# Optimization experiments

Measured on AMD Instinct MI355X. Metric: run time of the kernel, lower is better.

The kernel has to match this reference:

```python
import jax, jax.numpy as jnp
import numpy as np

EPS = 1e-10


def setup_inputs() -> dict:
    key = jax.random.key(0)
    k1, k2, k3 = jax.random.split(key, 3)
    B, c = 65536, 64
    xyz = jax.random.normal(k1, (B, 3, 1), dtype=jnp.float32)          # group centers
    xyz_group = xyz + 0.1 * jax.random.normal(k2, (B, 3, c), dtype=jnp.float32)  # neighbor points
    r_lrf = 0.2 + 0.8 * jax.random.uniform(k3, (B,), dtype=jnp.float32)  # per-group support radius
    return {"xyz": xyz, "xyz_group": xyz_group, "r_lrf": r_lrf}


def reference(xyz, xyz_group, r_lrf):
    # xyz: [B,3,1] center; xyz_group: [B,3,c] neighbors; r_lrf: [B]
    B, _, c = xyz_group.shape
    x = xyz - xyz_group                                   # [B,3,c]
    xxt = jnp.einsum('bic,bjc->bij', x, x) / c            # [B,3,3] covariance
    _, _, vh = jnp.linalg.svd(xxt)                        # vh: [B,3,3]
    v_last = vh[:, -1, :]                                 # [B,3] smallest singular vector (torch v[...,-1])

    # sign disambiguation (no-grad in the original)
    center_proj = jnp.einsum('bi,bic->bc', v_last, x)     # [B,c]
    sum_ = (center_proj > 0.001).sum(-1) - (center_proj < -0.001).sum(-1)  # [B]
    sign = jax.lax.stop_gradient(1.0 - 2.0 * (sum_ < 0).astype(jnp.float32))  # [B]

    zp = sign[:, None] * v_last                           # [B,3] z axis
    x = -x                                                # x *= -1 in original
    norm = jnp.einsum('bi,bic->bc', zp, x)                # [B,c] projection onto zp
    vi = x - zp[:, :, None] * norm[:, None, :]            # [B,3,c] in-plane component
    x_l2 = jnp.sqrt(jnp.sum(x * x, axis=1))               # [B,c]
    alpha = (r_lrf[:, None] - x_l2) ** 2                  # [B,c]
    beta = norm * norm                                    # [B,c]
    vi_c = jnp.einsum('bc,bic->bi', alpha * beta, vi)     # [B,3] weighted sum
    xp = vi_c / (jnp.sqrt(jnp.sum(vi_c * vi_c, axis=1, keepdims=True)) + EPS)  # [B,3] x axis
    yp = jnp.cross(xp, zp)                                # [B,3] y axis
    lrf = jnp.stack([xp, yp, zp], axis=2)                 # [B,3,3] columns = axes
    out = jnp.einsum('bij,bic->bjc', lrf, (xyz_group - xyz) / r_lrf[:, None, None])  # lrf^T @ _out_xp
    return out


if __name__ == '__main__':
    o = reference(**setup_inputs())
    print(o.shape)
```

## Files before the change

### kernel.cpp

```cpp
#include <hip/hip_runtime.h>


#define DEVFN static __device__ __forceinline__


DEVFN float slapy2f(float x, float y) {
#pragma clang fp contract(off)
  float xa = fabsf(x), ya = fabsf(y);
  float w = fmaxf(xa, ya);
  float z = fminf(xa, ya);
  if (z == 0.0f) return w;
  float q = z / w;
  return w * sqrtf(fmaf(q, q, 1.0f));
}

DEVFN float snrm2_2f(float a, float b) {
  double da = (double)a, db = (double)b;
  return (float)sqrt(da * da + db * db);
}

DEVFN void slartgf(float f, float g, float &cs, float &sn, float &r) {
#pragma clang fp contract(off)
  if (g == 0.0f) { cs = 1.0f; sn = 0.0f; r = f; return; }
  if (f == 0.0f) { cs = 0.0f; sn = copysignf(1.0f, g); r = fabsf(g); return; }
  float f1 = fabsf(f), g1 = fabsf(g);
  const float rtmin = 0x1p-63f;
  const float rtmax = 6.5219089e18f;
  if (f1 > rtmin && f1 < rtmax && g1 > rtmin && g1 < rtmax) {
    float d = sqrtf(fmaf(f, f, g * g));
    cs = f1 / d;
    r = copysignf(d, f);
    sn = g / r;
  } else {
    const float safmin = 0x1p-126f;
    const float safmax = 0x1p+126f;
    float u = fminf(safmax, fmaxf(safmin, fmaxf(f1, g1)));
    float fs = f / u, gs = g / u;
    float d = sqrtf(fmaf(fs, fs, gs * gs));
    cs = fabsf(fs) / d;
    r = copysignf(d, f);
    sn = gs / r;
    r = r * u;
  }
}

DEVFN void slas2f(float f, float g, float h, float &ssmin, float &ssmax) {
#pragma clang fp contract(off)
  float fa = fabsf(f), ga = fabsf(g), ha = fabsf(h);
  float fhmn = fminf(fa, ha), fhmx = fmaxf(fa, ha);
  if (fhmn == 0.0f) {
    ssmin = 0.0f;
    if (fhmx == 0.0f) {
      ssmax = ga;
    } else {
      float mx = fmaxf(fhmx, ga), mn = fminf(fhmx, ga);
      float q = mn / mx;
      ssmax = mx * sqrtf(fmaf(q, q, 1.0f));
    }
  } else {
    if (ga < fhmx) {
      float as = 1.0f + fhmn / fhmx;
      float at = (fhmx - fhmn) / fhmx;
      float qq = ga / fhmx;
      float au = qq * qq;
      float c = 2.0f / (sqrtf(fmaf(as, as, au)) + sqrtf(fmaf(at, at, au)));
      ssmin = fhmn * c;
      ssmax = fhmx / c;
    } else {
      float au = fhmx / ga;
      if (au == 0.0f) {
        ssmin = (fhmn * fhmx) / ga;
        ssmax = ga;
      } else {
        float as = 1.0f + fhmn / fhmx;
        float at = (fhmx - fhmn) / fhmx;
        float q1 = as * au, q2 = at * au;
        float c = 1.0f / (sqrtf(fmaf(q1, q1, 1.0f)) + sqrtf(fmaf(q2, q2, 1.0f)));
        ssmin = (fhmn * c) * au;
        ssmin = ssmin + ssmin;
        ssmax = ga / (c + c);
      }
    }
  }
}

DEVFN void slasv2f(float f, float g, float h, float &ssmin, float &ssmax,
                   float &snr, float &csr, float &snl, float &csl) {
#pragma clang fp contract(off)
  const float eps = 0x1p-24f;
  float ft = f, fa = fabsf(f), ht = h, ha = fabsf(h);
  int pmax = 1;
  bool swp = (ha > fa);
  if (swp) {
    pmax = 3;
    float tmp = ft; ft = ht; ht = tmp;
    tmp = fa; fa = ha; ha = tmp;
  }
  float gt = g, ga = fabsf(g);
  float clt = 0.0f, crt = 0.0f, slt = 0.0f, srt = 0.0f;
  if (ga == 0.0f) {
    ssmin = ha; ssmax = fa;
    clt = 1.0f; crt = 1.0f; slt = 0.0f; srt = 0.0f;
  } else {
    bool gasmal = true;
    if (ga > fa) {
      pmax = 2;
      if ((fa / ga) < eps) {
        gasmal = false;
        ssmax = ga;
        if (ha > 1.0f) ssmin = fa / (ga / ha);
        else ssmin = (fa / ga) * ha;
        clt = 1.0f; slt = ht / gt; srt = 1.0f; crt = ft / gt;
      }
    }
    if (gasmal) {
      float dd = fa - ha;
      float l;
      if (dd == fa) l = 1.0f;
      else l = dd / fa;
      float m = gt / ft;
      float t = 2.0f - l;
      float s = sqrtf(fmaf(m, m, t * t));
      float r;
      if (l == 0.0f) r = fabsf(m);
      else r = sqrtf(fmaf(m, m, l * l));
      float a = 0.5f * (s + r);
      ssmin = ha / a;
      ssmax = fa * a;
      float mm = m * m;
      if (mm == 0.0f) {
        if (l == 0.0f) t = copysignf(2.0f, ft) * copysignf(1.0f, gt);
        else t = gt / copysignf(dd, ft) + m / t;
      } else {
        t = (m / (s + t) + m / (r + l)) * (1.0f + a);
      }
      float l2 = sqrtf(fmaf(t, t, 4.0f));
      crt = 2.0f / l2;
      srt = t / l2;
      clt = fmaf(srt, m, crt) / a;
      slt = (ht / ft) * srt / a;
    }
  }
  if (swp) { csl = srt; snl = crt; csr = slt; snr = clt; }
  else { csl = clt; snl = slt; csr = crt; snr = srt; }
  float tsign = 0.0f;
  if (pmax == 1) tsign = copysignf(1.0f, csr) * copysignf(1.0f, csl) * copysignf(1.0f, f);
  if (pmax == 2) tsign = copysignf(1.0f, snr) * copysignf(1.0f, csl) * copysignf(1.0f, g);
  if (pmax == 3) tsign = copysignf(1.0f, snr) * copysignf(1.0f, snl) * copysignf(1.0f, h);
  ssmax = copysignf(ssmax, tsign);
  ssmin = copysignf(ssmin, tsign * copysignf(1.0f, f) * copysignf(1.0f, h));
}

#define GROT(hi1, hi2, hi3, lo1, lo2, lo3, ct_, st_)          \
  do {                                                        \
    float c__ = (ct_), s__ = (st_);                           \
    if (c__ != 1.0f || s__ != 0.0f) {                         \
      float t_;                                               \
      t_ = hi1; hi1 = fmaf(c__, t_, -(s__ * lo1)); lo1 = fmaf(s__, t_, c__ * lo1); \
      t_ = hi2; hi2 = fmaf(c__, t_, -(s__ * lo2)); lo2 = fmaf(s__, t_, c__ * lo2); \
      t_ = hi3; hi3 = fmaf(c__, t_, -(s__ * lo3)); lo3 = fmaf(s__, t_, c__ * lo3); \
    }                                                         \
  } while (0)

#define ROT2X2(lo1, lo2, lo3, hi1, hi2, hi3, cr_, sr_)        \
  do {                                                        \
    float xx_, yy_, st_;                                      \
    xx_ = lo1; yy_ = hi1; st_ = fmaf(cr_, xx_, sr_ * yy_);    \
    hi1 = fmaf(cr_, yy_, -(sr_ * xx_)); lo1 = st_;            \
    xx_ = lo2; yy_ = hi2; st_ = fmaf(cr_, xx_, sr_ * yy_);    \
    hi2 = fmaf(cr_, yy_, -(sr_ * xx_)); lo2 = st_;            \
    xx_ = lo3; yy_ = hi3; st_ = fmaf(cr_, xx_, sr_ * yy_);    \
    hi3 = fmaf(cr_, yy_, -(sr_ * xx_)); lo3 = st_;            \
  } while (0)

#define VSWAP(a, b) { float t_ = (a); (a) = (b); (b) = t_; }

static __device__ void svd3_vlast(float c00, float c01, float c02,
                                  float c11, float c12, float c22,
                                  float vout[3]) {
#pragma clang fp contract(off)
  float a11 = c00, a12 = c01, a13 = c02;
  float a21 = c01, a22 = c11, a23 = c12;
  float a31 = c02, a32 = c12, a33 = c22;
  float d1, d2, d3, e1, e2;
  float taup1 = 0.0f, g2 = 0.0f;

  {
    float xnorm = snrm2_2f(a21, a31);
    if (xnorm == 0.0f) {
      d1 = a11;
    } else {
      float beta = -copysignf(slapy2f(a11, xnorm), a11);
      float tauq1 = (beta - a11) / beta;
      float sc = 1.0f / (a11 - beta);
      float v2 = a21 * sc, v3 = a31 * sc;
      d1 = beta;
      float w2 = fmaf(a32, v3, a22 * v2);
      float w3 = fmaf(a33, v3, a23 * v2);
      w2 = w2 + a12;
      w3 = w3 + a13;
      a12 = fmaf(-tauq1, w2, a12);
      a13 = fmaf(-tauq1, w3, a13);
      float t2 = -tauq1 * w2;
      float t3 = -tauq1 * w3;
      a22 = fmaf(v2, t2, a22); a32 = fmaf(v3, t2, a32);
      a23 = fmaf(v2, t3, a23); a33 = fmaf(v3, t3, a33);
    }
  }
  {
    float xnorm = fabsf(a13);
    if (xnorm == 0.0f) {
      e1 = a12;
    } else {
      float beta = -copysignf(slapy2f(a12, xnorm), a12);
      taup1 = (beta - a12) / beta;
      g2 = a13 * (1.0f / (a12 - beta));
      e1 = beta;
      float w2 = a23 * g2;
      float w3 = a33 * g2;
      w2 = w2 + a22;
      w3 = w3 + a32;
      a22 = fmaf(-taup1, w2, a22);
      a32 = fmaf(-taup1, w3, a32);
      float tg = -taup1 * g2;
      a23 = fmaf(w2, tg, a23);
      a33 = fmaf(w3, tg, a33);
    }
  }
  {
    float xnorm = fabsf(a32);
    if (xnorm == 0.0f) {
      d2 = a22;
    } else {
      float beta = -copysignf(slapy2f(a22, xnorm), a22);
      float tauq2 = (beta - a22) / beta;
      float h3 = a32 * (1.0f / (a22 - beta));
      d2 = beta;
      float w = a33 * h3;
      w = w + a23;
      a23 = fmaf(-tauq2, w, a23);
      float tw = -tauq2 * w;
      a33 = fmaf(h3, tw, a33);
    }
  }
  e2 = a23;
  d3 = a33;

  float vt11 = 1.0f, vt12 = 0.0f, vt13 = 0.0f;
  float vt21 = 0.0f, vt22 = 1.0f, vt23 = 0.0f;
  float vt31 = 0.0f, vt32 = 0.0f, vt33 = 1.0f;

  const float eps = 0x1p-24f;
  const float unfl = 0x1p-126f;
  const float tol = 10.0f * eps;
  float thresh;
  {
    float sminoa = fabsf(d1);
    if (sminoa != 0.0f) {
      float mu = sminoa;
      mu = fabsf(d2) * (mu / (mu + fabsf(e1)));
      sminoa = fminf(sminoa, mu);
      if (sminoa != 0.0f) {
        mu = fabsf(d3) * (mu / (mu + fabsf(e2)));
        sminoa = fminf(sminoa, mu);
      }
    }
    sminoa = sminoa / sqrtf(3.0f);
    thresh = fmaxf(tol * sminoa, 6.0f * (3.0f * (3.0f * unfl)));
  }
  int mq = 3;
  int iterq = -1, iterdivn = 0;
  const int maxitdivn = 18;
  int oldll = -1, oldm = -1, idir = 0;
  float sminl = 0.0f;
  int guard = 0;

  while (true) {
    if (mq <= 1) break;
    if (++guard > 300) break;
    if (iterq >= 3) {
      iterq -= 3;
      iterdivn += 1;
      if (iterdivn >= maxitdivn) break;
    }
    if (mq == 2) {
      if (fabsf(e1) <= thresh) { e1 = 0.0f; mq = 1; continue; }
      float sigmn, sigmx, sinr, cosr, sinl, cosl;
      slasv2f(d1, e1, d2, sigmn, sigmx, sinr, cosr, sinl, cosl);
      d1 = sigmx; e1 = 0.0f; d2 = sigmn;
      ROT2X2(vt11, vt12, vt13, vt21, vt22, vt23, cosr, sinr);
      mq = 0;
      continue;
    }
    float smax = fabsf(d3);
    if (fabsf(e2) <= thresh) { e2 = 0.0f; mq = 2; continue; }
    smax = fmaxf(fmaxf(smax, fabsf(d2)), fabsf(e2));
    if (fabsf(e1) <= thresh) {
      e1 = 0.0f;
      float sigmn, sigmx, sinr, cosr, sinl, cosl;
      slasv2f(d2, e2, d3, sigmn, sigmx, sinr, cosr, sinl, cosl);
      d2 = sigmx; e2 = 0.0f; d3 = sigmn;
      ROT2X2(vt21, vt22, vt23, vt31, vt32, vt33, cosr, sinr);
      mq = 1;
      continue;
    }
    smax = fmaxf(fmaxf(smax, fabsf(d1)), fabsf(e1));
    if (1 > oldm || 3 < oldll)
      idir = (fabsf(d1) >= fabsf(d3)) ? 1 : 2;
    bool back = false;
    if (idir == 1) {
      if (fabsf(e2) <= tol * fabsf(d3)) { e2 = 0.0f; continue; }
      float mu = fabsf(d1);
      sminl = mu;
      if (fabsf(e1) <= tol * mu) { e1 = 0.0f; back = true; }
      else {
        mu = fabsf(d2) * (mu / (mu + fabsf(e1)));
        sminl = fminf(sminl, mu);
        if (fabsf(e2) <= tol * mu) { e2 = 0.0f; back = true; }
        else {
          mu = fabsf(d3) * (mu / (mu + fabsf(e2)));
          sminl = fminf(sminl, mu);
        }
      }
    } else {
      if (fabsf(e1) <= tol * fabsf(d1)) { e1 = 0.0f; continue; }
      float mu = fabsf(d3);
      sminl = mu;
      if (fabsf(e2) <= tol * mu) { e2 = 0.0f; back = true; }
      else {
        mu = fabsf(d2) * (mu / (mu + fabsf(e2)));
        sminl = fminf(sminl, mu);
        if (fabsf(e1) <= tol * mu) { e1 = 0.0f; back = true; }
        else {
          mu = fabsf(d1) * (mu / (mu + fabsf(e1)));
          sminl = fminf(sminl, mu);
        }
      }
    }
    if (back) continue;
    oldll = 1;
    oldm = 3;
    float shift = 0.0f;
    if (!((3.0f * tol) * (sminl / smax) <= fmaxf(eps, 0.01f * tol))) {
      float sll, rdum;
      if (idir == 1) { sll = fabsf(d1); slas2f(d2, e2, d3, shift, rdum); }
      else { sll = fabsf(d3); slas2f(d1, e1, d2, shift, rdum); }
      if (sll > 0.0f) {
        float q = shift / sll;
        if (q * q < eps) shift = 0.0f;
      }
    }
    iterq += 2;
    float rc0, rc1, rs0, rs1;
    if (shift == 0.0f) {
      if (idir == 1) {
        float cs = 1.0f, oldcs = 1.0f, sn = 0.0f, oldsn = 0.0f, rr = 0.0f;
        float fq = d1 * cs;
        slartgf(fq, e1, cs, sn, rr);
        float f2 = oldcs * rr;
        float g2q = d2 * sn;
        slartgf(f2, g2q, oldcs, oldsn, d1);
        rc0 = cs; rs0 = sn;
        fq = d2 * cs;
        slartgf(fq, e2, cs, sn, rr);
        e1 = oldsn * rr;
        f2 = oldcs * rr;
        g2q = d3 * sn;
        slartgf(f2, g2q, oldcs, oldsn, d2);
        rc1 = cs; rs1 = sn;
        float h = d3 * cs;
        d3 = h * oldcs;
        e2 = h * oldsn;
        GROT(vt21, vt22, vt23, vt11, vt12, vt13, rc0, rs0);
        GROT(vt31, vt32, vt33, vt21, vt22, vt23, rc1, rs1);
        if (fabsf(e2) <= thresh) e2 = 0.0f;
      } else {
        float cs = 1.0f, oldcs = 1.0f, sn = 0.0f, oldsn = 0.0f, rr = 0.0f;
        float fq = d3 * cs;
        slartgf(fq, e2, cs, sn, rr);
        float f2 = oldcs * rr;
        float g2q = d2 * sn;
        slartgf(f2, g2q, oldcs, oldsn, d3);
        rc1 = oldcs; rs1 = -oldsn;
        fq = d2 * cs;
        slartgf(fq, e1, cs, sn, rr);
        e2 = oldsn * rr;
        f2 = oldcs * rr;
        g2q = d1 * sn;
        slartgf(f2, g2q, oldcs, oldsn, d2);
        rc0 = oldcs; rs0 = -oldsn;
        float h = d1 * cs;
        d1 = h * oldcs;
        e1 = h * oldsn;
        GROT(vt31, vt32, vt33, vt21, vt22, vt23, rc1, rs1);
        GROT(vt21, vt22, vt23, vt11, vt12, vt13, rc0, rs0);
        if (fabsf(e1) <= thresh) e1 = 0.0f;
      }
    } else {
      if (idir == 1) {
        float fq = (fabsf(d1) - shift) * (copysignf(1.0f, d1) + shift / d1);
        float gq = e1;
        float cosr = 0, sinr = 0, cosl = 0, sinl = 0, rr = 0;
        slartgf(fq, gq, cosr, sinr, rr);
        fq = fmaf(cosr, d1, sinr * e1);
        e1 = fmaf(cosr, e1, -(sinr * d1));
        gq = sinr * d2;
        d2 = cosr * d2;
        slartgf(fq, gq, cosl, sinl, rr);
        d1 = rr;
        fq = fmaf(cosl, e1, sinl * d2);
        d2 = fmaf(cosl, d2, -(sinl * e1));
        gq = sinl * e2;
        e2 = cosl * e2;
        rc0 = cosr; rs0 = sinr;
        slartgf(fq, gq, cosr, sinr, rr);
        e1 = rr;
        fq = fmaf(cosr, d2, sinr * e2);
        e2 = fmaf(cosr, e2, -(sinr * d2));
        gq = sinr * d3;
        d3 = cosr * d3;
        slartgf(fq, gq, cosl, sinl, rr);
        d2 = rr;
        fq = fmaf(cosl, e2, sinl * d3);
        d3 = fmaf(cosl, d3, -(sinl * e2));
        rc1 = cosr; rs1 = sinr;
        e2 = fq;
        GROT(vt21, vt22, vt23, vt11, vt12, vt13, rc0, rs0);
        GROT(vt31, vt32, vt33, vt21, vt22, vt23, rc1, rs1);
        if (fabsf(e2) <= thresh) e2 = 0.0f;
      } else {
        float fq = (fabsf(d3) - shift) * (copysignf(1.0f, d3) + shift / d3);
        float gq = e2;
        float cosr = 0, sinr = 0, cosl = 0, sinl = 0, rr = 0;
        slartgf(fq, gq, cosr, sinr, rr);
        fq = fmaf(cosr, d3, sinr * e2);
        e2 = fmaf(cosr, e2, -(sinr * d3));
        gq = sinr * d2;
        d2 = cosr * d2;
        slartgf(fq, gq, cosl, sinl, rr);
        d3 = rr;
        fq = fmaf(cosl, e2, sinl * d2);
        d2 = fmaf(cosl, d2, -(sinl * e2));
        gq = sinl * e1;
        e1 = cosl * e1;
        rc1 = cosl; rs1 = -sinl;
        slartgf(fq, gq, cosr, sinr, rr);
        e2 = rr;
        fq = fmaf(cosr, d2, sinr * e1);
        e1 = fmaf(cosr, e1, -(sinr * d2));
        gq = sinr * d1;
        d1 = cosr * d1;
        slartgf(fq, gq, cosl, sinl, rr);
        d2 = rr;
        fq = fmaf(cosl, e1, sinl * d1);
        d1 = fmaf(cosl, d1, -(sinl * e1));
        rc0 = cosl; rs0 = -sinl;
        e1 = fq;
        if (fabsf(e1) <= thresh) e1 = 0.0f;
        GROT(vt31, vt32, vt33, vt21, vt22, vt23, rc1, rs1);
        GROT(vt21, vt22, vt23, vt11, vt12, vt13, rc0, rs0);
      }
    }
  }
  if (d1 < 0.0f) { d1 = -d1; vt11 = -vt11; vt12 = -vt12; vt13 = -vt13; }
  if (d2 < 0.0f) { d2 = -d2; vt21 = -vt21; vt22 = -vt22; vt23 = -vt23; }
  if (d3 < 0.0f) { d3 = -d3; vt31 = -vt31; vt32 = -vt32; vt33 = -vt33; }
  {
    int isub = 1; float smin = d1;
    if (d2 <= smin) { isub = 2; smin = d2; }
    if (d3 <= smin) { isub = 3; smin = d3; }
    if (isub != 3) {
      if (isub == 1) {
        d1 = d3; d3 = smin;
        VSWAP(vt11, vt31); VSWAP(vt12, vt32); VSWAP(vt13, vt33);
      } else {
        d2 = d3; d3 = smin;
        VSWAP(vt21, vt31); VSWAP(vt22, vt32); VSWAP(vt23, vt33);
      }
    }
  }
  {
    int isub = 1; float smin = d1;
    if (d2 <= smin) { isub = 2; smin = d2; }
    if (isub != 2) {
      d1 = d2; d2 = smin;
      VSWAP(vt11, vt21); VSWAP(vt12, vt22); VSWAP(vt13, vt23);
    }
  }
  float r1 = vt31, r2 = vt32, r3 = vt33;
  if (taup1 != 0.0f) {
    float w = r3 * g2;
    w = w + r2;
    r2 = fmaf(-taup1, w, r2);
    float tg = -taup1 * g2;
    r3 = fmaf(w, tg, r3);
  }
  vout[0] = r1;
  vout[1] = r2;
  vout[2] = r3;
}

DEVFN float qsum(float x) {
#pragma clang fp contract(off)
  float s = x + __shfl_xor(x, 1);
  return s + __shfl_xor(s, 2);
}
DEVFN int qsumi(int x) {
  int s = x + __shfl_xor(x, 1);
  return s + __shfl_xor(s, 2);
}

#define CHAIN4(acc, A, Bv)            \
  do {                                \
    float t_ = A[3] * Bv[3] + acc;    \
    t_ = A[2] * Bv[2] + t_;           \
    t_ = A[1] * Bv[1] + t_;           \
    acc = A[0] * Bv[0] + t_;          \
  } while (0)


__global__ __launch_bounds__(256)
__attribute__((amdgpu_waves_per_eu(2, 4)))
void LRF_70695161692718_kernel(
    const float* __restrict__ xyz, const float* __restrict__ xyzg,
    const float* __restrict__ rl, float* __restrict__ out, int B) {
#pragma clang fp contract(off)
  int tid = blockIdx.x * blockDim.x + threadIdx.x;
  int b = tid >> 2;
  int l = tid & 3;
  if (b >= B) return;
  const float* Xg = xyzg + (size_t)b * 192;
  float cx = xyz[3 * b + 0], cy = xyz[3 * b + 1], cz = xyz[3 * b + 2];
  float r = rl[b];

  float r0[16], r1[16], r2[16];
#pragma unroll
  for (int i = 0; i < 16; ++i) {
    int col = 4 * i + l;
    r0[i] = Xg[col];
    r1[i] = Xg[64 + col];
    r2[i] = Xg[128 + col];
  }

  float a00 = 0, a01 = 0, a02 = 0, a11 = 0, a12 = 0, a22 = 0;
#pragma unroll
  for (int Bk = 0; Bk < 4; ++Bk) {
    float x0[4], x1[4], x2[4];
#pragma unroll
    for (int j = 0; j < 4; ++j) {
      int i = 4 * Bk + j;
      x0[j] = cx - r0[i];
      x1[j] = cy - r1[i];
      x2[j] = cz - r2[i];
    }
    CHAIN4(a00, x0, x0);
    CHAIN4(a01, x0, x1);
    CHAIN4(a02, x0, x2);
    CHAIN4(a11, x1, x1);
    CHAIN4(a12, x1, x2);
    CHAIN4(a22, x2, x2);
  }
  a00 = qsum(a00) / 64.0f;
  a01 = qsum(a01) / 64.0f;
  a02 = qsum(a02) / 64.0f;
  a11 = qsum(a11) / 64.0f;
  a12 = qsum(a12) / 64.0f;
  a22 = qsum(a22) / 64.0f;

  float v[3];
  svd3_vlast(a00, a01, a02, a11, a12, a22, v);

  int npos = 0, nneg = 0;
#pragma unroll
  for (int i = 0; i < 16; ++i) {
    float x0 = cx - r0[i];
    float x1 = cy - r1[i];
    float x2 = cz - r2[i];
    float p = v[0] * x0;
    p = v[1] * x1 + p;
    p = v[2] * x2 + p;
    npos += (p > 0.001f) ? 1 : 0;
    nneg += (p < -0.001f) ? 1 : 0;
  }
  int sum_ = qsumi(npos) - qsumi(nneg);
  float sgn = (sum_ < 0) ? -1.0f : 1.0f;
  float zp0 = sgn * v[0], zp1 = sgn * v[1], zp2 = sgn * v[2];

  float vx = 0, vy = 0, vz = 0;
#pragma unroll
  for (int Bk = 0; Bk < 4; ++Bk) {
    float w[4], q0[4], q1[4], q2[4];
#pragma unroll
    for (int j = 0; j < 4; ++j) {
      int i = 4 * Bk + j;
      float y0 = r0[i] - cx;
      float y1 = r1[i] - cy;
      float y2 = r2[i] - cz;
      float nm = zp0 * y0;
      nm = zp1 * y1 + nm;
      nm = zp2 * y2 + nm;
      q0[j] = y0 - zp0 * nm;
      q1[j] = y1 - zp1 * nm;
      q2[j] = y2 - zp2 * nm;
      float ss = y0 * y0;
      ss = ss + y1 * y1;
      ss = ss + y2 * y2;
      float xl2 = sqrtf(ss);
      float am = r - xl2;
      float alpha = am * am;
      float beta = nm * nm;
      w[j] = alpha * beta;
    }
    CHAIN4(vx, w, q0);
    CHAIN4(vy, w, q1);
    CHAIN4(vz, w, q2);
  }
  float vcx = qsum(vx);
  float vcy = qsum(vy);
  float vcz = qsum(vz);
  float ss = vcx * vcx;
  ss = ss + vcy * vcy;
  ss = ss + vcz * vcz;
  float den = sqrtf(ss) + 1e-10f;
  float xp0 = vcx / den, xp1 = vcy / den, xp2 = vcz / den;
  float yp0 = xp1 * zp2 - xp2 * zp1;
  float yp1 = xp2 * zp0 - xp0 * zp2;
  float yp2 = xp0 * zp1 - xp1 * zp0;

  float* O = out + (size_t)b * 192;
#pragma unroll
  for (int i = 0; i < 16; ++i) {
    int col = 4 * i + l;
    float y0 = r0[i] - cx;
    float y1 = r1[i] - cy;
    float y2 = r2[i] - cz;
    float p0 = y0 / r, p1 = y1 / r, p2 = y2 / r;
    float t0 = xp0 * p0; t0 = xp1 * p1 + t0; t0 = xp2 * p2 + t0;
    float t1 = yp0 * p0; t1 = yp1 * p1 + t1; t1 = yp2 * p2 + t1;
    float t2 = zp0 * p0; t2 = zp1 * p1 + t2; t2 = zp2 * p2 + t2;
    O[col] = t0;
    O[64 + col] = t1;
    O[128 + col] = t2;
  }
}

extern "C" void kernel_launch(void* const* d_in, const int* in_sizes, int n_in,
                              void* d_out, int out_size, void* d_ws, size_t ws_size,
                              hipStream_t stream) {
  (void)n_in; (void)out_size; (void)d_ws; (void)ws_size;
  const float* xyz = (const float*)d_in[0];
  const float* xyzg = (const float*)d_in[1];
  const float* rl = (const float*)d_in[2];
  float* out = (float*)d_out;
  int B = in_sizes[2];
  int threads = 256;
  int blocks = (B * 4 + threads - 1) / threads;
  LRF_70695161692718_kernel<<<blocks, threads, 0, stream>>>(xyz, xyzg, rl, out, B);
}
```

Measured before the change: 141.6 us.

## Split covariance/SVD into a separate one-thread-per-group kernel

Moves the covariance accumulation and 3x3 SVD into a new kernel that runs one thread per group and reads the group with float4 loads. It writes the smallest singular vector to workspace, or into the output buffer if no workspace is available. The original kernel becomes a finish kernel that reads that vector and does the sign test and projection. This removes the 4x redundant SVD computation across lanes, at the cost of an extra launch and reading the input twice.

```diff
diff --git a/kernel.cpp b/kernel.cpp
--- a/kernel.cpp
+++ b/kernel.cpp
@@ -518,12 +518,81 @@
     acc = A[0] * Bv[0] + t_;          \
   } while (0)
 
+#define CH1C(acc, A, Bv, C)                     \
+  do {                                          \
+    float t_ = A[3].C * Bv[3].C + acc.C;        \
+    t_ = A[2].C * Bv[2].C + t_;                 \
+    t_ = A[1].C * Bv[1].C + t_;                 \
+    acc.C = A[0].C * Bv[0].C + t_;              \
+  } while (0)
+#define CHAIN4V(acc, A, Bv) \
+  do { CH1C(acc, A, Bv, x); CH1C(acc, A, Bv, y); CH1C(acc, A, Bv, z); CH1C(acc, A, Bv, w); } while (0)
+
+DEVFN float qsum4(const float4 &a) {
+#pragma clang fp contract(off)
+  float s01 = a.x + a.y;
+  float s23 = a.z + a.w;
+  return s01 + s23;
+}
+
+
+__global__ __launch_bounds__(64)
+__attribute__((amdgpu_waves_per_eu(1, 4)))
+void LRF_70695161692718_svd(
+    const float* __restrict__ xyz, const float* __restrict__ xyzg,
+    float* __restrict__ vws, int vstride, int B) {
+#pragma clang fp contract(off)
+  int b = blockIdx.x * blockDim.x + threadIdx.x;
+  if (b >= B) return;
+  const float4* G0 = (const float4*)(xyzg + (size_t)b * 192);
+  const float4* G1 = G0 + 16;
+  const float4* G2 = G0 + 32;
+  float cx = xyz[3 * b + 0], cy = xyz[3 * b + 1], cz = xyz[3 * b + 2];
+
+  float4 a00 = {0, 0, 0, 0}, a01 = {0, 0, 0, 0}, a02 = {0, 0, 0, 0};
+  float4 a11 = {0, 0, 0, 0}, a12 = {0, 0, 0, 0}, a22 = {0, 0, 0, 0};
+#pragma unroll
+  for (int Bk = 0; Bk < 4; ++Bk) {
+    float4 x0[4], x1[4], x2[4];
+#pragma unroll
+    for (int j = 0; j < 4; ++j) {
+      float4 g0 = G0[4 * Bk + j];
+      float4 g1 = G1[4 * Bk + j];
+      float4 g2 = G2[4 * Bk + j];
+      x0[j].x = cx - g0.x; x0[j].y = cx - g0.y; x0[j].z = cx - g0.z; x0[j].w = cx - g0.w;
+      x1[j].x = cy - g1.x; x1[j].y = cy - g1.y; x1[j].z = cy - g1.z; x1[j].w = cy - g1.w;
+      x2[j].x = cz - g2.x; x2[j].y = cz - g2.y; x2[j].z = cz - g2.z; x2[j].w = cz - g2.w;
+    }
+    CHAIN4V(a00, x0, x0);
+    CHAIN4V(a01, x0, x1);
+    CHAIN4V(a02, x0, x2);
+    CHAIN4V(a11, x1, x1);
+    CHAIN4V(a12, x1, x2);
+    CHAIN4V(a22, x2, x2);
+  }
+  float c00 = qsum4(a00) / 64.0f;
+  float c01 = qsum4(a01) / 64.0f;
+  float c02 = qsum4(a02) / 64.0f;
+  float c11 = qsum4(a11) / 64.0f;
+  float c12 = qsum4(a12) / 64.0f;
+  float c22 = qsum4(a22) / 64.0f;
+
+  float v[3];
+  svd3_vlast(c00, c01, c02, c11, c12, c22, v);
+
+  float* vp = vws + (size_t)b * vstride;
+  vp[0] = v[0];
+  vp[1] = v[1];
+  vp[2] = v[2];
+}
+
 
 __global__ __launch_bounds__(256)
 __attribute__((amdgpu_waves_per_eu(2, 4)))
-void LRF_70695161692718_kernel(
+void LRF_70695161692718_finish(
     const float* __restrict__ xyz, const float* __restrict__ xyzg,
-    const float* __restrict__ rl, float* __restrict__ out, int B) {
+    const float* __restrict__ rl, const float* vws, int vstride,
+    float* out, int B) {
 #pragma clang fp contract(off)
   int tid = blockIdx.x * blockDim.x + threadIdx.x;
   int b = tid >> 2;
@@ -533,6 +602,12 @@
   float cx = xyz[3 * b + 0], cy = xyz[3 * b + 1], cz = xyz[3 * b + 2];
   float r = rl[b];
 
+  const float* vp = vws + (size_t)b * vstride;
+  float v[3];
+  v[0] = vp[0];
+  v[1] = vp[1];
+  v[2] = vp[2];
+
   float r0[16], r1[16], r2[16];
 #pragma unroll
   for (int i = 0; i < 16; ++i) {
@@ -541,34 +616,6 @@
     r1[i] = Xg[64 + col];
     r2[i] = Xg[128 + col];
   }
-
-  float a00 = 0, a01 = 0, a02 = 0, a11 = 0, a12 = 0, a22 = 0;
-#pragma unroll
-  for (int Bk = 0; Bk < 4; ++Bk) {
-    float x0[4], x1[4], x2[4];
-#pragma unroll
-    for (int j = 0; j < 4; ++j) {
-      int i = 4 * Bk + j;
-      x0[j] = cx - r0[i];
-      x1[j] = cy - r1[i];
-      x2[j] = cz - r2[i];
-    }
-    CHAIN4(a00, x0, x0);
-    CHAIN4(a01, x0, x1);
-    CHAIN4(a02, x0, x2);
-    CHAIN4(a11, x1, x1);
-    CHAIN4(a12, x1, x2);
-    CHAIN4(a22, x2, x2);
-  }
-  a00 = qsum(a00) / 64.0f;
-  a01 = qsum(a01) / 64.0f;
-  a02 = qsum(a02) / 64.0f;
-  a11 = qsum(a11) / 64.0f;
-  a12 = qsum(a12) / 64.0f;
-  a22 = qsum(a22) / 64.0f;
-
-  float v[3];
-  svd3_vlast(a00, a01, a02, a11, a12, a22, v);
 
   int npos = 0, nneg = 0;
 #pragma unroll
@@ -647,13 +694,24 @@
 extern "C" void kernel_launch(void* const* d_in, const int* in_sizes, int n_in,
                               void* d_out, int out_size, void* d_ws, size_t ws_size,
                               hipStream_t stream) {
-  (void)n_in; (void)out_size; (void)d_ws; (void)ws_size;
+  (void)n_in; (void)out_size;
   const float* xyz = (const float*)d_in[0];
   const float* xyzg = (const float*)d_in[1];
   const float* rl = (const float*)d_in[2];
   float* out = (float*)d_out;
   int B = in_sizes[2];
-  int threads = 256;
-  int blocks = (B * 4 + threads - 1) / threads;
-  LRF_70695161692718_kernel<<<blocks, threads, 0, stream>>>(xyz, xyzg, rl, out, B);
-}
+
+  float* vws;
+  int vstride;
+  if (d_ws != nullptr && ws_size >= (size_t)B * 3 * sizeof(float)) {
+    vws = (float*)d_ws;
+    vstride = 3;
+  } else {
+    vws = out;
+    vstride = 192;
+  }
+
+  LRF_70695161692718_svd<<<(B + 63) / 64, 64, 0, stream>>>(xyz, xyzg, vws, vstride, B);
+  LRF_70695161692718_finish<<<(B * 4 + 255) / 256, 256, 0, stream>>>(
+      xyz, xyzg, rl, vws, vstride, out, B);
+}
```

Measured after the change: 143.4 us. About the same (+1.2%).

## Use fast double Jacobi eigensolver with fallback LAPACK-style path for ill-conditioned groups

Applied to the files above, without the earlier changes.

The main kernel replaces the bit-exact LAPACK-style SVD emulation with a 4-sweep double-precision Jacobi eigensolver. It flags groups whose eigen-gap is small, whose sign vote is near a threshold, or whose x-axis is sensitive to a perturbed z-axis, and saves their covariance to workspace. A second kernel recomputes only the flagged groups with the original SVD path and overwrites their output. The perturbation check needs an extra weighted pass, the second launch rereads the flag array, and there is a risk of mismatches when the heuristics miss an ill-conditioned case.

```diff
diff --git a/kernel.cpp b/kernel.cpp
--- a/kernel.cpp
+++ b/kernel.cpp
@@ -500,6 +500,87 @@
   vout[2] = r3;
 }
 
+
+#define JSWAP(a, b) { double t_ = (a); (a) = (b); (b) = t_; }
+
+DEVFN void jacobi3(float c00f, float c01f, float c02f,
+                   float c11f, float c12f, float c22f,
+                   float vmin[3], float u2o[3], double &lmax, double &gap) {
+  double a00 = (double)c00f, a01 = (double)c01f, a02 = (double)c02f;
+  double a11 = (double)c11f, a12 = (double)c12f, a22 = (double)c22f;
+  double v00 = 1.0, v01 = 0.0, v02 = 0.0;
+  double v10 = 0.0, v11 = 1.0, v12 = 0.0;
+  double v20 = 0.0, v21 = 0.0, v22 = 1.0;
+
+#pragma unroll
+  for (int sweep = 0; sweep < 4; ++sweep) {
+    if (a01 != 0.0) {
+      double tau = (a11 - a00) / (2.0 * a01);
+      double t = (tau >= 0.0 ? 1.0 : -1.0) / (fabs(tau) + sqrt(1.0 + tau * tau));
+      double c = 1.0 / sqrt(1.0 + t * t);
+      double s = t * c;
+      a00 = a00 - t * a01;
+      a11 = a11 + t * a01;
+      a01 = 0.0;
+      double n02 = c * a02 - s * a12;
+      double n12 = s * a02 + c * a12;
+      a02 = n02; a12 = n12;
+      double x;
+      x = v00; v00 = c * x - s * v01; v01 = s * x + c * v01;
+      x = v10; v10 = c * x - s * v11; v11 = s * x + c * v11;
+      x = v20; v20 = c * x - s * v21; v21 = s * x + c * v21;
+    }
+    if (a02 != 0.0) {
+      double tau = (a22 - a00) / (2.0 * a02);
+      double t = (tau >= 0.0 ? 1.0 : -1.0) / (fabs(tau) + sqrt(1.0 + tau * tau));
+      double c = 1.0 / sqrt(1.0 + t * t);
+      double s = t * c;
+      a00 = a00 - t * a02;
+      a22 = a22 + t * a02;
+      a02 = 0.0;
+      double n01 = c * a01 - s * a12;
+      double n12 = s * a01 + c * a12;
+      a01 = n01; a12 = n12;
+      double x;
+      x = v00; v00 = c * x - s * v02; v02 = s * x + c * v02;
+      x = v10; v10 = c * x - s * v12; v12 = s * x + c * v12;
+      x = v20; v20 = c * x - s * v22; v22 = s * x + c * v22;
+    }
+    if (a12 != 0.0) {
+      double tau = (a22 - a11) / (2.0 * a12);
+      double t = (tau >= 0.0 ? 1.0 : -1.0) / (fabs(tau) + sqrt(1.0 + tau * tau));
+      double c = 1.0 / sqrt(1.0 + t * t);
+      double s = t * c;
+      a11 = a11 - t * a12;
+      a22 = a22 + t * a12;
+      a12 = 0.0;
+      double n01 = c * a01 - s * a02;
+      double n02 = s * a01 + c * a02;
+      a01 = n01; a02 = n02;
+      double x;
+      x = v01; v01 = c * x - s * v02; v02 = s * x + c * v02;
+      x = v11; v11 = c * x - s * v12; v12 = s * x + c * v12;
+      x = v21; v21 = c * x - s * v22; v22 = s * x + c * v22;
+    }
+  }
+
+  double L0 = a00, L1 = a11, L2 = a22;
+  if (L0 < L1) { JSWAP(L0, L1); JSWAP(v00, v01); JSWAP(v10, v11); JSWAP(v20, v21); }
+  if (L0 < L2) { JSWAP(L0, L2); JSWAP(v00, v02); JSWAP(v10, v12); JSWAP(v20, v22); }
+  if (L1 < L2) { JSWAP(L1, L2); JSWAP(v01, v02); JSWAP(v11, v12); JSWAP(v21, v22); }
+  lmax = L0;
+  gap = L1 - L2;
+
+  double n2 = 1.0 / sqrt(v02 * v02 + v12 * v12 + v22 * v22);
+  vmin[0] = (float)(v02 * n2);
+  vmin[1] = (float)(v12 * n2);
+  vmin[2] = (float)(v22 * n2);
+  double n1 = 1.0 / sqrt(v01 * v01 + v11 * v11 + v21 * v21);
+  u2o[0] = (float)(v01 * n1);
+  u2o[1] = (float)(v11 * n1);
+  u2o[2] = (float)(v21 * n1);
+}
+
 DEVFN float qsum(float x) {
 #pragma clang fp contract(off)
   float s = x + __shfl_xor(x, 1);
@@ -518,12 +599,49 @@
     acc = A[0] * Bv[0] + t_;          \
   } while (0)
 
+#define PASS3(Z0, Z1, Z2, OVX, OVY, OVZ)                      \
+  do {                                                        \
+    float vx = 0, vy = 0, vz = 0;                             \
+    _Pragma("unroll")                                         \
+    for (int Bk = 0; Bk < 4; ++Bk) {                          \
+      float w[4], q0[4], q1[4], q2[4];                        \
+      _Pragma("unroll")                                       \
+      for (int j = 0; j < 4; ++j) {                           \
+        int i = 4 * Bk + j;                                   \
+        float y0 = r0[i] - cx;                                \
+        float y1 = r1[i] - cy;                                \
+        float y2 = r2[i] - cz;                                \
+        float nm = (Z0) * y0;                                 \
+        nm = (Z1) * y1 + nm;                                  \
+        nm = (Z2) * y2 + nm;                                  \
+        q0[j] = y0 - (Z0) * nm;                               \
+        q1[j] = y1 - (Z1) * nm;                               \
+        q2[j] = y2 - (Z2) * nm;                               \
+        float ss_ = y0 * y0;                                  \
+        ss_ = ss_ + y1 * y1;                                  \
+        ss_ = ss_ + y2 * y2;                                  \
+        float xl2_ = sqrtf(ss_);                              \
+        float am_ = r - xl2_;                                 \
+        float alpha_ = am_ * am_;                             \
+        float beta_ = nm * nm;                                \
+        w[j] = alpha_ * beta_;                                \
+      }                                                       \
+      CHAIN4(vx, w, q0);                                      \
+      CHAIN4(vy, w, q1);                                      \
+      CHAIN4(vz, w, q2);                                      \
+    }                                                         \
+    OVX = qsum(vx);                                           \
+    OVY = qsum(vy);                                           \
+    OVZ = qsum(vz);                                           \
+  } while (0)
+
 
 __global__ __launch_bounds__(256)
 __attribute__((amdgpu_waves_per_eu(2, 4)))
-void LRF_70695161692718_kernel(
+void LRF_70695161692718_main(
     const float* __restrict__ xyz, const float* __restrict__ xyzg,
-    const float* __restrict__ rl, float* __restrict__ out, int B) {
+    const float* __restrict__ rl, float* __restrict__ out,
+    float* __restrict__ ws, int B) {
 #pragma clang fp contract(off)
   int tid = blockIdx.x * blockDim.x + threadIdx.x;
   int b = tid >> 2;
@@ -567,10 +685,14 @@
   a12 = qsum(a12) / 64.0f;
   a22 = qsum(a22) / 64.0f;
 
-  float v[3];
-  svd3_vlast(a00, a01, a02, a11, a12, a22, v);
-
-  int npos = 0, nneg = 0;
+  float v[3], u2[3];
+  double lmax, gap;
+  jacobi3(a00, a01, a02, a11, a12, a22, v, u2, lmax, gap);
+
+  int flag = !(gap > 0.032 * lmax);
+
+  const float MARG = 3.1e-5f;
+  int npos = 0, nneg = 0, nshk = 0;
 #pragma unroll
   for (int i = 0; i < 16; ++i) {
     float x0 = cx - r0[i];
@@ -579,50 +701,46 @@
     float p = v[0] * x0;
     p = v[1] * x1 + p;
     p = v[2] * x2 + p;
+    float ss_ = x0 * x0;
+    ss_ = ss_ + x1 * x1;
+    ss_ = ss_ + x2 * x2;
+    float xl2_ = sqrtf(ss_);
     npos += (p > 0.001f) ? 1 : 0;
     nneg += (p < -0.001f) ? 1 : 0;
+    nshk += (fabsf(fabsf(p) - 0.001f) <= MARG * xl2_) ? 1 : 0;
   }
   int sum_ = qsumi(npos) - qsumi(nneg);
+  int nsh = qsumi(nshk);
+  flag |= (sum_ >= -nsh) && (sum_ <= nsh);
+
   float sgn = (sum_ < 0) ? -1.0f : 1.0f;
   float zp0 = sgn * v[0], zp1 = sgn * v[1], zp2 = sgn * v[2];
 
-  float vx = 0, vy = 0, vz = 0;
-#pragma unroll
-  for (int Bk = 0; Bk < 4; ++Bk) {
-    float w[4], q0[4], q1[4], q2[4];
-#pragma unroll
-    for (int j = 0; j < 4; ++j) {
-      int i = 4 * Bk + j;
-      float y0 = r0[i] - cx;
-      float y1 = r1[i] - cy;
-      float y2 = r2[i] - cz;
-      float nm = zp0 * y0;
-      nm = zp1 * y1 + nm;
-      nm = zp2 * y2 + nm;
-      q0[j] = y0 - zp0 * nm;
-      q1[j] = y1 - zp1 * nm;
-      q2[j] = y2 - zp2 * nm;
-      float ss = y0 * y0;
-      ss = ss + y1 * y1;
-      ss = ss + y2 * y2;
-      float xl2 = sqrtf(ss);
-      float am = r - xl2;
-      float alpha = am * am;
-      float beta = nm * nm;
-      w[j] = alpha * beta;
-    }
-    CHAIN4(vx, w, q0);
-    CHAIN4(vy, w, q1);
-    CHAIN4(vz, w, q2);
-  }
-  float vcx = qsum(vx);
-  float vcy = qsum(vy);
-  float vcz = qsum(vz);
+  float vcx, vcy, vcz;
+  PASS3(zp0, zp1, zp2, vcx, vcy, vcz);
+  float pz0 = sgn * (v[0] + 3e-5f * u2[0]);
+  float pz1 = sgn * (v[1] + 3e-5f * u2[1]);
+  float pz2 = sgn * (v[2] + 3e-5f * u2[2]);
+  float wcx, wcy, wcz;
+  PASS3(pz0, pz1, pz2, wcx, wcy, wcz);
+
   float ss = vcx * vcx;
   ss = ss + vcy * vcy;
   ss = ss + vcz * vcz;
-  float den = sqrtf(ss) + 1e-10f;
+  float vnorm = sqrtf(ss);
+  float den = vnorm + 1e-10f;
   float xp0 = vcx / den, xp1 = vcy / den, xp2 = vcz / den;
+
+  float ssp = wcx * wcx + wcy * wcy + wcz * wcz;
+  float denp = sqrtf(ssp) + 1e-10f;
+  float qp0 = wcx / denp, qp1 = wcy / denp, qp2 = wcz / denp;
+  float d0 = xp0 - qp0, d1 = xp1 - qp1, d2 = xp2 - qp2;
+  float d2sum = d0 * d0 + d1 * d1 + d2 * d2;
+  float dv0 = vcx - wcx, dv1 = vcy - wcy, dv2 = vcz - wcz;
+  float dvic2 = dv0 * dv0 + dv1 * dv1 + dv2 * dv2;
+  flag |= !(d2sum < 1.2e-5f);
+  flag |= !(vnorm * vnorm > 900.0f * dvic2);
+
   float yp0 = xp1 * zp2 - xp2 * zp1;
   float yp1 = xp2 * zp0 - xp0 * zp2;
   float yp2 = xp0 * zp1 - xp1 * zp0;
@@ -642,18 +760,207 @@
     O[64 + col] = t1;
     O[128 + col] = t2;
   }
+
+  if (l == 0) {
+    float* s = ws + (size_t)b * 8;
+    s[0] = flag ? 1.0f : 0.0f;
+    if (flag) {
+      s[1] = a00; s[2] = a01; s[3] = a02;
+      s[4] = a11; s[5] = a12; s[6] = a22;
+    }
+  }
+}
+
+
+__global__ __launch_bounds__(256)
+__attribute__((amdgpu_waves_per_eu(2, 4)))
+void LRF_70695161692718_fix(
+    const float* __restrict__ xyz, const float* __restrict__ xyzg,
+    const float* __restrict__ rl, float* __restrict__ out,
+    const float* __restrict__ ws, int B) {
+#pragma clang fp contract(off)
+  int tid = blockIdx.x * blockDim.x + threadIdx.x;
+  int b = tid >> 2;
+  int l = tid & 3;
+  if (b >= B) return;
+  const float* s = ws + (size_t)b * 8;
+  if (s[0] == 0.0f) return;
+
+  float a00 = s[1], a01 = s[2], a02 = s[3];
+  float a11 = s[4], a12 = s[5], a22 = s[6];
+
+  float v[3];
+  svd3_vlast(a00, a01, a02, a11, a12, a22, v);
+
+  const float* Xg = xyzg + (size_t)b * 192;
+  float cx = xyz[3 * b + 0], cy = xyz[3 * b + 1], cz = xyz[3 * b + 2];
+  float r = rl[b];
+
+  float r0[16], r1[16], r2[16];
+#pragma unroll
+  for (int i = 0; i < 16; ++i) {
+    int col = 4 * i + l;
+    r0[i] = Xg[col];
+    r1[i] = Xg[64 + col];
+    r2[i] = Xg[128 + col];
+  }
+
+  int npos = 0, nneg = 0;
+#pragma unroll
+  for (int i = 0; i < 16; ++i) {
+    float x0 = cx - r0[i];
+    float x1 = cy - r1[i];
+    float x2 = cz - r2[i];
+    float p = v[0] * x0;
+    p = v[1] * x1 + p;
+    p = v[2] * x2 + p;
+    npos += (p > 0.001f) ? 1 : 0;
+    nneg += (p < -0.001f) ? 1 : 0;
+  }
+  int sum_ = qsumi(npos) - qsumi(nneg);
+  float sgn = (sum_ < 0) ? -1.0f : 1.0f;
+  float zp0 = sgn * v[0], zp1 = sgn * v[1], zp2 = sgn * v[2];
+
+  float vcx, vcy, vcz;
+  PASS3(zp0, zp1, zp2, vcx, vcy, vcz);
+  float ss = vcx * vcx;
+  ss = ss + vcy * vcy;
+  ss = ss + vcz * vcz;
+  float den = sqrtf(ss) + 1e-10f;
+  float xp0 = vcx / den, xp1 = vcy / den, xp2 = vcz / den;
+  float yp0 = xp1 * zp2 - xp2 * zp1;
+  float yp1 = xp2 * zp0 - xp0 * zp2;
+  float yp2 = xp0 * zp1 - xp1 * zp0;
+
+  float* O = out + (size_t)b * 192;
+#pragma unroll
+  for (int i = 0; i < 16; ++i) {
+    int col = 4 * i + l;
+    float y0 = r0[i] - cx;
+    float y1 = r1[i] - cy;
+    float y2 = r2[i] - cz;
+    float p0 = y0 / r, p1 = y1 / r, p2 = y2 / r;
+    float t0 = xp0 * p0; t0 = xp1 * p1 + t0; t0 = xp2 * p2 + t0;
+    float t1 = yp0 * p0; t1 = yp1 * p1 + t1; t1 = yp2 * p2 + t1;
+    float t2 = zp0 * p0; t2 = zp1 * p1 + t2; t2 = zp2 * p2 + t2;
+    O[col] = t0;
+    O[64 + col] = t1;
+    O[128 + col] = t2;
+  }
+}
+
+
+__global__ __launch_bounds__(256)
+__attribute__((amdgpu_waves_per_eu(2, 4)))
+void LRF_70695161692718_mono(
+    const float* __restrict__ xyz, const float* __restrict__ xyzg,
+    const float* __restrict__ rl, float* __restrict__ out, int B) {
+#pragma clang fp contract(off)
+  int tid = blockIdx.x * blockDim.x + threadIdx.x;
+  int b = tid >> 2;
+  int l = tid & 3;
+  if (b >= B) return;
+  const float* Xg = xyzg + (size_t)b * 192;
+  float cx = xyz[3 * b + 0], cy = xyz[3 * b + 1], cz = xyz[3 * b + 2];
+  float r = rl[b];
+
+  float r0[16], r1[16], r2[16];
+#pragma unroll
+  for (int i = 0; i < 16; ++i) {
+    int col = 4 * i + l;
+    r0[i] = Xg[col];
+    r1[i] = Xg[64 + col];
+    r2[i] = Xg[128 + col];
+  }
+
+  float a00 = 0, a01 = 0, a02 = 0, a11 = 0, a12 = 0, a22 = 0;
+#pragma unroll
+  for (int Bk = 0; Bk < 4; ++Bk) {
+    float x0[4], x1[4], x2[4];
+#pragma unroll
+    for (int j = 0; j < 4; ++j) {
+      int i = 4 * Bk + j;
+      x0[j] = cx - r0[i];
+      x1[j] = cy - r1[i];
+      x2[j] = cz - r2[i];
+    }
+    CHAIN4(a00, x0, x0);
+    CHAIN4(a01, x0, x1);
+    CHAIN4(a02, x0, x2);
+    CHAIN4(a11, x1, x1);
+    CHAIN4(a12, x1, x2);
+    CHAIN4(a22, x2, x2);
+  }
+  a00 = qsum(a00) / 64.0f;
+  a01 = qsum(a01) / 64.0f;
+  a02 = qsum(a02) / 64.0f;
+  a11 = qsum(a11) / 64.0f;
+  a12 = qsum(a12) / 64.0f;
+  a22 = qsum(a22) / 64.0f;
+
+  float v[3];
+  svd3_vlast(a00, a01, a02, a11, a12, a22, v);
+
+  int npos = 0, nneg = 0;
+#pragma unroll
+  for (int i = 0; i < 16; ++i) {
+    float x0 = cx - r0[i];
+    float x1 = cy - r1[i];
+    float x2 = cz - r2[i];
+    float p = v[0] * x0;
+    p = v[1] * x1 + p;
+    p = v[2] * x2 + p;
+    npos += (p > 0.001f) ? 1 : 0;
+    nneg += (p < -0.001f) ? 1 : 0;
+  }
+  int sum_ = qsumi(npos) - qsumi(nneg);
+  float sgn = (sum_ < 0) ? -1.0f : 1.0f;
+  float zp0 = sgn * v[0], zp1 = sgn * v[1], zp2 = sgn * v[2];
+
+  float vcx, vcy, vcz;
+  PASS3(zp0, zp1, zp2, vcx, vcy, vcz);
+  float ss = vcx * vcx;
+  ss = ss + vcy * vcy;
+  ss = ss + vcz * vcz;
+  float den = sqrtf(ss) + 1e-10f;
+  float xp0 = vcx / den, xp1 = vcy / den, xp2 = vcz / den;
+  float yp0 = xp1 * zp2 - xp2 * zp1;
+  float yp1 = xp2 * zp0 - xp0 * zp2;
+  float yp2 = xp0 * zp1 - xp1 * zp0;
+
+  float* O = out + (size_t)b * 192;
+#pragma unroll
+  for (int i = 0; i < 16; ++i) {
+    int col = 4 * i + l;
+    float y0 = r0[i] - cx;
+    float y1 = r1[i] - cy;
+    float y2 = r2[i] - cz;
+    float p0 = y0 / r, p1 = y1 / r, p2 = y2 / r;
+    float t0 = xp0 * p0; t0 = xp1 * p1 + t0; t0 = xp2 * p2 + t0;
+    float t1 = yp0 * p0; t1 = yp1 * p1 + t1; t1 = yp2 * p2 + t1;
+    float t2 = zp0 * p0; t2 = zp1 * p1 + t2; t2 = zp2 * p2 + t2;
+    O[col] = t0;
+    O[64 + col] = t1;
+    O[128 + col] = t2;
+  }
 }
 
 extern "C" void kernel_launch(void* const* d_in, const int* in_sizes, int n_in,
                               void* d_out, int out_size, void* d_ws, size_t ws_size,
                               hipStream_t stream) {
-  (void)n_in; (void)out_size; (void)d_ws; (void)ws_size;
+  (void)n_in; (void)out_size;
   const float* xyz = (const float*)d_in[0];
   const float* xyzg = (const float*)d_in[1];
   const float* rl = (const float*)d_in[2];
   float* out = (float*)d_out;
   int B = in_sizes[2];
-  int threads = 256;
-  int blocks = (B * 4 + threads - 1) / threads;
-  LRF_70695161692718_kernel<<<blocks, threads, 0, stream>>>(xyz, xyzg, rl, out, B);
-}
+  int blocks = (B * 4 + 255) / 256;
+
+  if (d_ws != nullptr && ws_size >= (size_t)B * 32) {
+    float* ws = (float*)d_ws;
+    LRF_70695161692718_main<<<blocks, 256, 0, stream>>>(xyz, xyzg, rl, out, ws, B);
+    LRF_70695161692718_fix<<<blocks, 256, 0, stream>>>(xyz, xyzg, rl, out, ws, B);
+  } else {
+    LRF_70695161692718_mono<<<blocks, 256, 0, stream>>>(xyz, xyzg, rl, out, B);
+  }
+}
```

New measurement: 177.0 us. +25.0%, slower.
